# Kernel optimization log

Measured on AMD Instinct MI355X. Metric: run time of the kernel, lower is better.

Reference implementation:

```python
import jax, jax.numpy as jnp
import numpy as np

THRESHOLD = 0.5  # default threshold from MemoryPool.update

N, D, P, C0 = 16384, 1024, 4096, 2048


def setup_inputs() -> dict:
    key = jax.random.key(0)
    k1, k2, k3, k4 = jax.random.split(key, 4)
    summaries = jax.random.normal(k1, (N, D), dtype=jnp.float32)
    scores = jax.random.uniform(k2, (N,), dtype=jnp.float32)
    slot = jnp.arange(P)
    # slots >= count are empty (zeros), matching fresh torch buffers
    pool = jnp.where((slot < C0)[:, None],
                     jax.random.normal(k3, (P, D), dtype=jnp.float32), 0.0)
    priorities = jnp.where(slot < C0,
                           jax.random.uniform(k4, (P,), dtype=jnp.float32), 0.0)
    return {"summaries": summaries, "scores": scores,
            "pool": pool, "priorities": priorities, "count": C0}


def reference(summaries, scores, pool, priorities, count):
    pool_size = pool.shape[0]
    cnt0 = jnp.asarray(count, jnp.int32)

    def step(carry, xc):
        pl, pr, cnt = carry
        s, sc = xc  # (D,), ()
        valid = sc > THRESHOLD
        min_idx = jnp.argmin(pr)
        has_room = cnt < pool_size
        idx = jnp.where(has_room, cnt, min_idx)
        replace_ok = sc > pr[min_idx]
        do_write = valid & (has_room | replace_ok)
        new_pl = jnp.where(do_write, pl.at[idx].set(s), pl)
        new_pr = jnp.where(do_write, pr.at[idx].set(sc), pr)
        new_cnt = cnt + (do_write & has_room).astype(jnp.int32)
        return (new_pl, new_pr, new_cnt), None

    (pool_out, prior_out, cnt_out), _ = jax.lax.scan(
        step, (pool, priorities, cnt0), (summaries, scores))
    return pool_out, prior_out, cnt_out
```

## Files before the change

kernel.cpp:

```cpp
#include <hip/hip_runtime.h>

typedef unsigned long long u64;
#define THRESH 0.5f
#define ALL1 0xFFFFFFFFFFFFFFFFull
#define FINF __builtin_inff()

__device__ __forceinline__ u64 shflxU64(u64 v, int m) { return __shfl_xor(v, m, 64); }
__device__ __forceinline__ void sort64(u64 &key, int lane) {
#pragma unroll
    for (int k = 2; k <= 64; k <<= 1) {
#pragma unroll
        for (int j = k >> 1; j > 0; j >>= 1) {
            u64 p = shflxU64(key, j);
            bool takeMax = ((lane & j) != 0) != ((lane & k) != 0);
            u64 mn = key < p ? key : p;
            u64 mx = key < p ? p : key;
            key = takeMax ? mx : mn;
        }
    }
}

__device__ __forceinline__ u64 mkey(float v, int id) {
    v = (v == 0.0f) ? 0.0f : v;
    unsigned u = __float_as_uint(v);
    u ^= (unsigned)((int)u >> 31) | 0x80000000u;
    return ((u64)u << 32) | (unsigned)id;
}

__device__ __forceinline__ int blockScanExcl1024(int c, int tid, int* wpart,
                                                 int* totalOut) {
    const int lane = tid & 63, wid = tid >> 6;
    int pc = c;
#pragma unroll
    for (int off = 1; off < 64; off <<= 1) {
        int y = __shfl_up(pc, off, 64);
        if (lane >= off) pc += y;
    }
    if (lane == 63) wpart[wid] = pc;
    __syncthreads();
    if (tid < 16) {
        int v = wpart[tid];
#pragma unroll
        for (int off = 1; off < 16; off <<= 1) {
            int y = __shfl_up(v, off, 16);
            if (tid >= off) v += y;
        }
        wpart[tid] = v;
    }
    __syncthreads();
    *totalOut = wpart[15];
    return pc - c + (wid > 0 ? wpart[wid - 1] : 0);
}

__global__ __launch_bounds__(1024) void k1_scan(
    const float* __restrict__ scores, const float* __restrict__ priorities,
    const int* __restrict__ countPtr, int N, int P,
    float* __restrict__ outPrior, float* __restrict__ outCnt, int* __restrict__ srcWs,
    float* __restrict__ cval, int* __restrict__ csrc, int* __restrict__ meta,
    int* __restrict__ cnt2, int* __restrict__ cnt4)
{
    const int tid = threadIdx.x;
    for (int s = tid; s < P; s += 1024) { outPrior[s] = priorities[s]; srcWs[s] = -1; }
    for (int s = tid; s < N; s += 1024) cnt2[s] = 0;
    for (int s = tid; s < P + N; s += 1024) cnt4[s] = 0;
    int C0 = *countPtr; C0 = C0 < 0 ? 0 : (C0 > P ? P : C0);
    const int per = (N + 1023) >> 10;
    const int i0 = tid * per;
    float sv[16];
    if (per == 16 && i0 + 16 <= N) {
        const float4* s4 = (const float4*)(scores + i0);
        const float4 a = s4[0], b = s4[1], c4 = s4[2], d = s4[3];
        sv[0]=a.x; sv[1]=a.y; sv[2]=a.z; sv[3]=a.w;
        sv[4]=b.x; sv[5]=b.y; sv[6]=b.z; sv[7]=b.w;
        sv[8]=c4.x; sv[9]=c4.y; sv[10]=c4.z; sv[11]=c4.w;
        sv[12]=d.x; sv[13]=d.y; sv[14]=d.z; sv[15]=d.w;
    } else {
#pragma unroll 16
        for (int j = 0; j < 16; ++j)
            sv[j] = (j < per && i0 + j < N) ? scores[i0 + j] : 0.f;
    }
    int c = 0;
#pragma unroll 16
    for (int j = 0; j < 16; ++j) c += (j < per && i0 + j < N && sv[j] > THRESH) ? 1 : 0;
    __shared__ int wpart[16];
    int total;
    int v = blockScanExcl1024(c, tid, wpart, &total);
    int A = P - C0; if (A > total) A = total; if (A < 0) A = 0;
#pragma unroll 16
    for (int j = 0; j < 16; ++j) {
        if (j < per && i0 + j < N) {
            const float sc = sv[j];
            if (sc > THRESH) {
                if (v < A) { outPrior[C0 + v] = sc; srcWs[C0 + v] = i0 + j; }
                else { cval[v - A] = sc; csrc[v - A] = i0 + j; }
                ++v;
            }
        }
    }
    if (tid == 0) {
        meta[0] = total - A;
        meta[1] = C0 + A;
        outCnt[0] = (float)(C0 + A);
    }
}

#define K2T 512
__global__ __launch_bounds__(256) void k2_count(
    const float* __restrict__ outPrior, const float* __restrict__ cval,
    const int* __restrict__ meta, int* __restrict__ cnt2)
{
    const int M = meta[0], F = meta[1];
    const int iB = blockIdx.x << 8;
    if (iB >= M) return;
    const int hi = min(M, iB + 256);
    const int smax = F + hi;
    const int tb = blockIdx.y * K2T;
    if (tb >= smax) return;
    const int te = min(smax - tb, K2T);
    __shared__ __align__(16) float tile[K2T];
    for (int t = threadIdx.x; t < K2T; t += 256) {
        const int s = tb + t;
        tile[t] = (t < te) ? ((s < F) ? outPrior[s] : cval[s - F]) : FINF;
    }
    __syncthreads();
    const int i = iB + threadIdx.x;
    if (i >= M) return;
    const float x = cval[i];
    int cnt = 0;
    const float4* t4 = (const float4*)tile;
    if (tb + K2T <= F + iB) {
#pragma unroll 8
        for (int q = 0; q < K2T / 4; ++q) {
            const float4 w = t4[q];
            cnt += (w.x < x) + (w.y < x) + (w.z < x) + (w.w < x);
        }
    } else {
        int lim = F + i - tb;
        if (lim < 0) lim = 0;
        if (lim > te) lim = te;
        const int l4 = lim >> 2;
        for (int q = 0; q < l4; ++q) {
            const float4 w = t4[q];
            cnt += (w.x < x) + (w.y < x) + (w.z < x) + (w.w < x);
        }
        for (int t = l4 << 2; t < lim; ++t) cnt += tile[t] < x;
    }
    if (cnt) atomicAdd(&cnt2[i], cnt);
}

__global__ __launch_bounds__(1024) void k3_compact(
    const float* __restrict__ cval, const int* __restrict__ csrc,
    const int* __restrict__ cnt2, int* __restrict__ meta,
    float* __restrict__ cvalS, float* __restrict__ wval, int* __restrict__ wsrc,
    int* __restrict__ writeNum)
{
    const int M = meta[0];
    const int tid = threadIdx.x;
    const int per = (M + 1023) >> 10;
    const int i0 = tid * per, i1 = min(i0 + per, M);
    int c = 0;
    for (int i = i0; i < i1; ++i) c += (cnt2[i] >= i + 1) ? 1 : 0;
    __shared__ int wpart[16];
    int total;
    int w = blockScanExcl1024(c, tid, wpart, &total);
    for (int i = i0; i < i1; ++i) {
        if (cnt2[i] >= i + 1) {
            wval[w] = cval[i]; wsrc[w] = csrc[i]; writeNum[i] = w; cvalS[i] = cval[i]; ++w;
        } else { writeNum[i] = -1; cvalS[i] = FINF; }
    }
    if (tid == 0) meta[2] = total;
}

#define K4T 512
__global__ __launch_bounds__(256) void k4_count(
    const float* __restrict__ outPrior, const float* __restrict__ cvalS,
    const int* __restrict__ meta, int P, int* __restrict__ cnt4)
{
    const int M = meta[0], F = meta[1];
    if (M == 0) return;
    const int tot = F + M;
    const int eB = blockIdx.x << 8;
    if (eB >= tot) return;
    const int tb = blockIdx.y * K4T;
    if (tb >= tot) return;
    const int te = min(tot - tb, K4T);
    __shared__ __align__(16) u64 tile[K4T];
    for (int t = threadIdx.x; t < K4T; t += 256) {
        const int s = tb + t;
        u64 kk = ALL1;
        if (t < te) {
            if (s < F) kk = mkey(outPrior[s], s);
            else       kk = mkey(cvalS[s - F], P + (s - F));
        }
        tile[t] = kk;
    }
    __syncthreads();
    const int e = eB + threadIdx.x;
    if (e >= tot) return;
    float x; int id;
    if (e < F) { x = outPrior[e]; id = e; }
    else {
        x = cvalS[e - F];
        if (x == FINF) return;
        id = P + (e - F);
    }
    const u64 kx = mkey(x, id);
    int cnt = 0;
    const ulonglong2* t2 = (const ulonglong2*)tile;
#pragma unroll 8
    for (int q = 0; q < K4T / 2; ++q) {
        const ulonglong2 w = t2[q];
        cnt += (int)(w.x < kx) + (int)(w.y < kx);
    }
    if (cnt) atomicAdd(&cnt4[e], cnt);
}

#define SCAP 14400
#define DONEF (1 << 30)
#define MSF   (1 << 29)
#define TIEF  (1 << 28)
#define RSF   (1 << 27)
#define PAYM  ((1 << 27) - 1)
__global__ __launch_bounds__(1024) void k5_chain(
    float* __restrict__ evV, int* __restrict__ evId,
    const int* __restrict__ meta, int P,
    const float* __restrict__ wval, const int* __restrict__ wsrc,
    int* __restrict__ survW,
    float* outPrior, int* __restrict__ srcWs,
    const float* __restrict__ cvalS, const int* __restrict__ writeNum,
    const int* __restrict__ cnt4)
{
    __shared__ int state[SCAP];
    __shared__ int shRp, shLeft;
    const int tid = threadIdx.x;
    const int M = meta[0], F = meta[1], R = meta[2];
    if (M == 0) return;
    const int tot = F + M;

    for (int e = tid; e < tot; e += 1024) {
        float x; int myid; bool isC = false; int wn = -1;
        if (e < F) { x = outPrior[e]; myid = e; }
        else {
            const int i = e - F;
            x = cvalS[i];
            if (x == FINF) continue;
            isC = true; wn = writeNum[i]; myid = P + i;
        }
        const int cnt = cnt4[e];
        if (isC) survW[wn] = (cnt >= R) ? 1 : 0;
        if (cnt < R + 64) { evV[cnt] = x; evId[cnt] = isC ? (P + wn) : myid; }
    }
    __syncthreads();

    if (R <= 0 || R > SCAP) return;
    const int Wtot = F + R;

    if (tid == 0) {
        int Rp = R;
        if (R < Wtot) {
            const float vR1 = evV[R - 1];
            if (evV[R] == vR1) {
                int rr = R - 1;
                while (rr >= 0 && evV[rr] == vR1) --rr;
                Rp = rr + 1;
            }
        }
        shRp = Rp;
    }
    __syncthreads();
    const int Rp = shRp;

    for (int r = tid; r < Rp; r += 1024) {
        const float v = evV[r];
        const bool tp = (r > 0) && (evV[r - 1] == v);
        const bool tn = (r + 1 < Rp) && (evV[r + 1] == v);
        const bool tie = tp || tn;
        const int rs = (tie && !tp) ? RSF : 0;
        const int id = evId[r];
        int st;
        if (id < P) st = id | MSF | (tie ? (TIEF | rs) : DONEF);
        else        st = (id - P) | (tie ? (TIEF | rs) : 0);
        state[r] = st;
    }
    __syncthreads();

    for (int round = 0; round < Rp + 2; ++round) {
        for (int r = tid; r < Rp; r += 1024) {
            const int s = state[r];
            if (s & MSF) continue;
            int p = s & PAYM;
            int ms = -1;
            for (int g = 0; g < Rp + 2; ++g) {
                const int sp = state[p];
                if (sp & DONEF) { ms = sp & PAYM; break; }
                if (sp & (MSF | TIEF)) break;
                const int q = sp & PAYM;
                if (q >= p) break;
                p = q;
            }
            if (ms >= 0)
                state[r] = ms | MSF | ((s & TIEF) ? (s & (TIEF | RSF)) : DONEF);
            else
                state[r] = p | (s & (TIEF | RSF));
        }
        __syncthreads();
        for (int r = tid; r < Rp; r += 1024) {
            const int s = state[r];
            if (!(s & RSF) || (s & DONEF)) continue;
            int re = r + 1;
            while (re < Rp) {
                const int t = state[re];
                if ((t & TIEF) && !(t & RSF)) ++re; else break;
            }
            bool ready = true;
            for (int q = r; q < re; ++q) ready &= (state[q] & MSF) != 0;
            if (!ready) continue;
            for (int j = r; j < re; ++j) {
                int best = j;
                for (int q = j + 1; q < re; ++q)
                    if ((state[q] & PAYM) < (state[best] & PAYM)) best = q;
                if (best != j) {
                    const int pj = state[j] & PAYM, pb = state[best] & PAYM;
                    state[j]    = (state[j] & ~PAYM) | pb;
                    state[best] = (state[best] & ~PAYM) | pj;
                }
            }
            for (int j = r; j < re; ++j) state[j] |= DONEF;
        }
        __syncthreads();
        if (tid == 0) shLeft = 0;
        __syncthreads();
        int loc = 0;
        for (int r = tid; r < Rp; r += 1024) loc += (state[r] & DONEF) ? 0 : 1;
        if (loc) atomicAdd(&shLeft, loc);
        __syncthreads();
        if (shLeft == 0) break;
    }
    __syncthreads();

    if (Rp < R && tid < 64) {
        const int lane = tid;
        const int r = Rp + lane;
        const float v0 = evV[Rp];
        const bool mem = (r < Wtot) && (evV[r] == v0);
        const int g = (int)__popcll(__ballot(mem));
        const int e = R - Rp;
        int id = 0, ms = 0;
        if (mem) {
            id = evId[r];
            ms = (id < P) ? id : (state[id - P] & PAYM);
        }
        u64 key = mem ? ((((u64)(unsigned)ms) << 32) | (u64)(unsigned)id) : ALL1;
        sort64(key, lane);
        const int sid = (int)(unsigned)(key & 0xFFFFFFFFull);
        const int sms = (int)(unsigned)(key >> 32);
        const bool real = (key != ALL1) && (lane < g);
        if (real && lane < e) state[Rp + lane] = sms;
        if (real && sid >= P) survW[sid - P] = (lane >= e) ? 1 : 0;
    }
    __syncthreads();

    for (int j = tid; j < R; j += 1024) {
        if (survW[j]) {
            const int sl = state[j] & PAYM;
            outPrior[sl] = wval[j];
            srcWs[sl] = wsrc[j];
        }
    }
}

__global__ __launch_bounds__(256) void gather_kernel(
    const float* __restrict__ summaries,
    const float* __restrict__ pool,
    const int* __restrict__ src,
    float* __restrict__ outPool, int D) {
    int p = blockIdx.x;
    int s = src[p];
    const float* row = (s >= 0) ? (summaries + (size_t)s * D) : (pool + (size_t)p * D);
    float* o = outPool + (size_t)p * D;
    if ((D & 3) == 0) {
        for (int k = (threadIdx.x << 2); k < D; k += (blockDim.x << 2)) {
            float4 v = *(const float4*)(row + k);
            *(float4*)(o + k) = v;
        }
    } else {
        for (int k = threadIdx.x; k < D; k += blockDim.x) o[k] = row[k];
    }
}

extern "C" void kernel_launch(void* const* d_in, const int* in_sizes, int n_in,
                              void* d_out, int out_size, void* d_ws, size_t ws_size,
                              hipStream_t stream) {
    const float* summaries  = (const float*)d_in[0];
    const float* scores     = (const float*)d_in[1];
    const float* pool       = (const float*)d_in[2];
    const float* priorities = (const float*)d_in[3];
    const int*   count      = (const int*)d_in[4];

    int N = in_sizes[1];
    int P = in_sizes[3];
    int D = in_sizes[0] / N;

    float* outPool  = (float*)d_out;
    float* outPrior = outPool + (size_t)P * D;
    float* outCnt   = outPrior + P;
    int*   srcWs    = (int*)d_ws;

    float* cval     = outPool;
    int*   csrc     = (int*)outPool + 1 * N;
    float* cvalS    = outPool + 3 * N;
    float* wval     = outPool + 4 * N;
    int*   wsrc     = (int*)outPool + 5 * N;
    int*   writeNum = (int*)outPool + 6 * N;
    float* evV      = outPool + 7 * N;
    int*   evId     = (int*)outPool + 8 * N + 64;
    int*   survW    = (int*)outPool + 10 * N + 128;
    int*   meta     = (int*)outPool + 11 * N + 128;
    int*   cnt2     = (int*)outPool + 11 * N + 192;
    int*   cnt4     = (int*)outPool + 12 * N + 192;

    const int nb2 = (N + 255) / 256;
    const int nb4 = (P + N + 255) / 256;
    const int ty  = (P + N + K2T - 1) / K2T;

    dim3 g2(nb2, ty), g4(nb4, ty);

    k1_scan<<<1, 1024, 0, stream>>>(scores, priorities, count, N, P,
                                    outPrior, outCnt, srcWs, cval, csrc, meta,
                                    cnt2, cnt4);
    k2_count<<<g2, 256, 0, stream>>>(outPrior, cval, meta, cnt2);
    k3_compact<<<1, 1024, 0, stream>>>(cval, csrc, cnt2, meta, cvalS, wval, wsrc, writeNum);
    k4_count<<<g4, 256, 0, stream>>>(outPrior, cvalS, meta, P, cnt4);
    k5_chain<<<1, 1024, 0, stream>>>(evV, evId, meta, P, wval, wsrc, survW,
                                     outPrior, srcWs, cvalS, writeNum, cnt4);
    gather_kernel<<<P, 256, 0, stream>>>(summaries, pool, srcWs, outPool, D);
}
```

Before: 183.9 us.

## Fuse count and compact kernels via ticket, move scatter into k4, parallelize init

Spreads the buffer initialisation in k1 across 16 extra blocks, and has the single scan block fill only the untouched prior slots. k2 and k3 become one kernel: the last block to finish, picked with an atomic ticket counter, does the compaction. k4 packs a per-element completion count into the high bits of its atomic counter, so whichever block finishes an element also scatters evV/evId/survW, removing that serial loop from the single-block k5. The gather becomes a grid-stride loop over 1024 blocks. The aim is fewer launches and less single-block serial work, at the cost of atomic-ticket ordering subtleties, and tickets is reset by k1 blocks that run concurrently with block 0.

```diff
diff --git a/kernel.cpp b/kernel.cpp
--- a/kernel.cpp
+++ b/kernel.cpp
@@ -4,6 +4,9 @@
 #define THRESH 0.5f
 #define ALL1 0xFFFFFFFFFFFFFFFFull
 #define FINF __builtin_inff()
+
+#define TOUCHB (1 << 20)
+#define CMASK  (TOUCHB - 1)
 
 __device__ __forceinline__ u64 shflxU64(u64 v, int m) { return __shfl_xor(v, m, 64); }
 __device__ __forceinline__ void sort64(u64 &key, int lane) {
@@ -57,13 +60,21 @@
     const int* __restrict__ countPtr, int N, int P,
     float* __restrict__ outPrior, float* __restrict__ outCnt, int* __restrict__ srcWs,
     float* __restrict__ cval, int* __restrict__ csrc, int* __restrict__ meta,
-    int* __restrict__ cnt2, int* __restrict__ cnt4)
+    int* __restrict__ cnt2, int* __restrict__ cnt4, int* __restrict__ tickets)
 {
     const int tid = threadIdx.x;
-    for (int s = tid; s < P; s += 1024) { outPrior[s] = priorities[s]; srcWs[s] = -1; }
-    for (int s = tid; s < N; s += 1024) cnt2[s] = 0;
-    for (int s = tid; s < P + N; s += 1024) cnt4[s] = 0;
     int C0 = *countPtr; C0 = C0 < 0 ? 0 : (C0 > P ? P : C0);
+
+    if (blockIdx.x != 0) {
+        const int bt = (int)(blockIdx.x - 1) * 1024 + tid;
+        const int BT = 16 * 1024;
+        for (int s = bt; s < C0; s += BT) { outPrior[s] = priorities[s]; srcWs[s] = -1; }
+        for (int s = bt; s < N; s += BT) cnt2[s] = 0;
+        for (int s = bt; s < P + N; s += BT) cnt4[s] = 0;
+        if (bt == 0) tickets[0] = 0;
+        return;
+    }
+
     const int per = (N + 1023) >> 10;
     const int i0 = tid * per;
     float sv[16];
@@ -97,6 +108,9 @@
             }
         }
     }
+    for (int s = C0 + A + tid; s < P; s += 1024) {
+        outPrior[s] = priorities[s]; srcWs[s] = -1;
+    }
     if (tid == 0) {
         meta[0] = total - A;
         meta[1] = C0 + A;
@@ -105,66 +119,78 @@
 }
 
 #define K2T 512
-__global__ __launch_bounds__(256) void k2_count(
+__global__ __launch_bounds__(1024) void k23(
     const float* __restrict__ outPrior, const float* __restrict__ cval,
-    const int* __restrict__ meta, int* __restrict__ cnt2)
-{
-    const int M = meta[0], F = meta[1];
-    const int iB = blockIdx.x << 8;
-    if (iB >= M) return;
-    const int hi = min(M, iB + 256);
-    const int smax = F + hi;
-    const int tb = blockIdx.y * K2T;
-    if (tb >= smax) return;
-    const int te = min(smax - tb, K2T);
-    __shared__ __align__(16) float tile[K2T];
-    for (int t = threadIdx.x; t < K2T; t += 256) {
-        const int s = tb + t;
-        tile[t] = (t < te) ? ((s < F) ? outPrior[s] : cval[s - F]) : FINF;
-    }
-    __syncthreads();
-    const int i = iB + threadIdx.x;
-    if (i >= M) return;
-    const float x = cval[i];
-    int cnt = 0;
-    const float4* t4 = (const float4*)tile;
-    if (tb + K2T <= F + iB) {
-#pragma unroll 8
-        for (int q = 0; q < K2T / 4; ++q) {
-            const float4 w = t4[q];
-            cnt += (w.x < x) + (w.y < x) + (w.z < x) + (w.w < x);
-        }
-    } else {
-        int lim = F + i - tb;
-        if (lim < 0) lim = 0;
-        if (lim > te) lim = te;
-        const int l4 = lim >> 2;
-        for (int q = 0; q < l4; ++q) {
-            const float4 w = t4[q];
-            cnt += (w.x < x) + (w.y < x) + (w.z < x) + (w.w < x);
-        }
-        for (int t = l4 << 2; t < lim; ++t) cnt += tile[t] < x;
-    }
-    if (cnt) atomicAdd(&cnt2[i], cnt);
-}
-
-__global__ __launch_bounds__(1024) void k3_compact(
-    const float* __restrict__ cval, const int* __restrict__ csrc,
-    const int* __restrict__ cnt2, int* __restrict__ meta,
+    const int* __restrict__ csrc, int* __restrict__ meta,
+    int* __restrict__ cnt2, int* __restrict__ tickets,
     float* __restrict__ cvalS, float* __restrict__ wval, int* __restrict__ wsrc,
     int* __restrict__ writeNum)
 {
-    const int M = meta[0];
+    __shared__ __align__(16) float tile[K2T];
+    __shared__ int wpart[16];
+    __shared__ int shLast;
     const int tid = threadIdx.x;
+    const int M = meta[0], F = meta[1];
+
+    const int iB = (int)blockIdx.x << 10;
+    const int tb = (int)blockIdx.y * K2T;
+    int te = 0;
+    if (iB < M) {
+        const int hi = min(M, iB + 1024);
+        const int smax = F + hi;
+        if (tb < smax) te = min(smax - tb, K2T);
+    }
+    if (te > 0) {
+        for (int t = tid; t < K2T; t += 1024) {
+            const int s = tb + t;
+            tile[t] = (t < te) ? ((s < F) ? outPrior[s] : cval[s - F]) : FINF;
+        }
+        __syncthreads();
+        const int i = iB + tid;
+        if (i < M) {
+            const float x = cval[i];
+            int cnt = 0;
+            const float4* t4 = (const float4*)tile;
+            if (tb + K2T <= F + iB) {
+#pragma unroll 8
+                for (int q = 0; q < K2T / 4; ++q) {
+                    const float4 w = t4[q];
+                    cnt += (w.x < x) + (w.y < x) + (w.z < x) + (w.w < x);
+                }
+            } else {
+                int lim = F + i - tb;
+                if (lim < 0) lim = 0;
+                if (lim > te) lim = te;
+                const int l4 = lim >> 2;
+                for (int q = 0; q < l4; ++q) {
+                    const float4 w = t4[q];
+                    cnt += (w.x < x) + (w.y < x) + (w.z < x) + (w.w < x);
+                }
+                for (int t = l4 << 2; t < lim; ++t) cnt += tile[t] < x;
+            }
+            if (cnt) atomicAdd(&cnt2[i], cnt);
+        }
+    }
+    __syncthreads();
+    if (tid == 0)
+        shLast = (atomicAdd(&tickets[0], 1) == (int)(gridDim.x * gridDim.y) - 1);
+    __syncthreads();
+    if (!shLast) return;
+
     const int per = (M + 1023) >> 10;
     const int i0 = tid * per, i1 = min(i0 + per, M);
+    int cv[16];
     int c = 0;
-    for (int i = i0; i < i1; ++i) c += (cnt2[i] >= i + 1) ? 1 : 0;
-    __shared__ int wpart[16];
+    for (int i = i0, j = 0; i < i1; ++i, ++j) {
+        const int q = atomicAdd(&cnt2[i], 0);
+        cv[j] = q;
+        c += (q >= i + 1) ? 1 : 0;
+    }
+    __syncthreads();
     int total;
     int w = blockScanExcl1024(c, tid, wpart, &total);
-    for (int i = i0; i < i1; ++i) {
-        if (cnt2[i] >= i + 1) {
+    for (int i = i0, j = 0; i < i1; ++i, ++j) {
+        if (cv[j] >= i + 1) {
             wval[w] = cval[i]; wsrc[w] = csrc[i]; writeNum[i] = w; cvalS[i] = cval[i]; ++w;
         } else { writeNum[i] = -1; cvalS[i] = FINF; }
     }
@@ -174,14 +200,16 @@
 #define K4T 512
 __global__ __launch_bounds__(256) void k4_count(
     const float* __restrict__ outPrior, const float* __restrict__ cvalS,
-    const int* __restrict__ meta, int P, int* __restrict__ cnt4)
+    const int* __restrict__ writeNum, const int* __restrict__ meta, int P,
+    int* __restrict__ cnt4,
+    float* __restrict__ evV, int* __restrict__ evId, int* __restrict__ survW)
 {
     const int M = meta[0], F = meta[1];
     if (M == 0) return;
     const int tot = F + M;
-    const int eB = blockIdx.x << 8;
+    const int eB = (int)blockIdx.x << 8;
     if (eB >= tot) return;
-    const int tb = blockIdx.y * K4T;
+    const int tb = (int)blockIdx.y * K4T;
     if (tb >= tot) return;
     const int te = min(tot - tb, K4T);
     __shared__ __align__(16) u64 tile[K4T];
@@ -197,12 +225,12 @@
     __syncthreads();
     const int e = eB + threadIdx.x;
     if (e >= tot) return;
-    float x; int id;
+    float x; int id; bool isC = false;
     if (e < F) { x = outPrior[e]; id = e; }
     else {
         x = cvalS[e - F];
         if (x == FINF) return;
-        id = P + (e - F);
+        id = P + (e - F); isC = true;
     }
     const u64 kx = mkey(x, id);
     int cnt = 0;
@@ -212,7 +240,19 @@
         const ulonglong2 w = t2[q];
         cnt += (int)(w.x < kx) + (int)(w.y < kx);
     }
-    if (cnt) atomicAdd(&cnt4[e], cnt);
+    const int TY = (tot + K4T - 1) / K4T;
+    const int old = atomicAdd(&cnt4[e], cnt | TOUCHB);
+    if ((old >> 20) == TY - 1) {
+        const int fin = (old & CMASK) + cnt;
+        const int R = meta[2];
+        if (isC) {
+            const int wn = writeNum[e - F];
+            survW[wn] = (fin >= R) ? 1 : 0;
+            if (fin < R + 64) { evV[fin] = x; evId[fin] = P + wn; }
+        } else {
+            if (fin < R + 64) { evV[fin] = x; evId[fin] = e; }
+        }
+    }
 }
 
 #define SCAP 14400
@@ -222,37 +262,18 @@
 #define RSF   (1 << 27)
 #define PAYM  ((1 << 27) - 1)
 __global__ __launch_bounds__(1024) void k5_chain(
-    float* __restrict__ evV, int* __restrict__ evId,
+    const float* __restrict__ evV, const int* __restrict__ evId,
     const int* __restrict__ meta, int P,
     const float* __restrict__ wval, const int* __restrict__ wsrc,
     int* __restrict__ survW,
-    float* outPrior, int* __restrict__ srcWs,
-    const float* __restrict__ cvalS, const int* __restrict__ writeNum,
-    const int* __restrict__ cnt4)
+    float* outPrior, int* __restrict__ srcWs)
 {
     __shared__ int state[SCAP];
     __shared__ int shRp, shLeft;
     const int tid = threadIdx.x;
-    const int M = meta[0], F = meta[1], R = meta[2];
-    if (M == 0) return;
-    const int tot = F + M;
-
-    for (int e = tid; e < tot; e += 1024) {
-        float x; int myid; bool isC = false; int wn = -1;
-        if (e < F) { x = outPrior[e]; myid = e; }
-        else {
-            const int i = e - F;
-            x = cvalS[i];
-            if (x == FINF) continue;
-            isC = true; wn = writeNum[i]; myid = P + i;
-        }
-        const int cnt = cnt4[e];
-        if (isC) survW[wn] = (cnt >= R) ? 1 : 0;
-        if (cnt < R + 64) { evV[cnt] = x; evId[cnt] = isC ? (P + wn) : myid; }
-    }
-    __syncthreads();
-
+    const int R = meta[2];
     if (R <= 0 || R > SCAP) return;
+    const int F = meta[1];
     const int Wtot = F + R;
 
     if (tid == 0) {
@@ -373,18 +394,19 @@
     const float* __restrict__ summaries,
     const float* __restrict__ pool,
     const int* __restrict__ src,
-    float* __restrict__ outPool, int D) {
-    int p = blockIdx.x;
-    int s = src[p];
-    const float* row = (s >= 0) ? (summaries + (size_t)s * D) : (pool + (size_t)p * D);
-    float* o = outPool + (size_t)p * D;
-    if ((D & 3) == 0) {
-        for (int k = (threadIdx.x << 2); k < D; k += (blockDim.x << 2)) {
-            float4 v = *(const float4*)(row + k);
-            *(float4*)(o + k) = v;
-        }
-    } else {
-        for (int k = threadIdx.x; k < D; k += blockDim.x) o[k] = row[k];
+    float* __restrict__ outPool, int P, int D) {
+    for (int p = blockIdx.x; p < P; p += gridDim.x) {
+        const int s = src[p];
+        const float* row = (s >= 0) ? (summaries + (size_t)s * D)
+                                    : (pool + (size_t)p * D);
+        float* o = outPool + (size_t)p * D;
+        if ((D & 3) == 0) {
+            const int dq = D >> 2;
+            for (int k = threadIdx.x; k < dq; k += blockDim.x)
+                ((float4*)o)[k] = ((const float4*)row)[k];
+        } else {
+            for (int k = threadIdx.x; k < D; k += blockDim.x) o[k] = row[k];
+        }
     }
 }
 
@@ -418,20 +440,20 @@
     int*   meta     = (int*)outPool + 11 * N + 128;
     int*   cnt2     = (int*)outPool + 11 * N + 192;
     int*   cnt4     = (int*)outPool + 12 * N + 192;
-
-    const int nb2 = (N + 255) / 256;
-    const int nb4 = (P + N + 255) / 256;
-    const int ty  = (P + N + K2T - 1) / K2T;
-
-    dim3 g2(nb2, ty), g4(nb4, ty);
-
-    k1_scan<<<1, 1024, 0, stream>>>(scores, priorities, count, N, P,
-                                    outPrior, outCnt, srcWs, cval, csrc, meta,
-                                    cnt2, cnt4);
-    k2_count<<<g2, 256, 0, stream>>>(outPrior, cval, meta, cnt2);
-    k3_compact<<<1, 1024, 0, stream>>>(cval, csrc, cnt2, meta, cvalS, wval, wsrc, writeNum);
-    k4_count<<<g4, 256, 0, stream>>>(outPrior, cvalS, meta, P, cnt4);
+    int*   tickets  = (int*)outPool + 13 * N + 256;
+
+    const int ty = (P + N + K2T - 1) / K2T;
+    dim3 g23((N + 1023) / 1024, ty);
+    dim3 g4((P + N + 255) / 256, ty);
+
+    k1_scan<<<17, 1024, 0, stream>>>(scores, priorities, count, N, P,
+                                     outPrior, outCnt, srcWs, cval, csrc, meta,
+                                     cnt2, cnt4, tickets);
+    k23<<<g23, 1024, 0, stream>>>(outPrior, cval, csrc, meta, cnt2, tickets,
+                                  cvalS, wval, wsrc, writeNum);
+    k4_count<<<g4, 256, 0, stream>>>(outPrior, cvalS, writeNum, meta, P, cnt4,
+                                     evV, evId, survW);
     k5_chain<<<1, 1024, 0, stream>>>(evV, evId, meta, P, wval, wsrc, survW,
-                                     outPrior, srcWs, cvalS, writeNum, cnt4);
-    gather_kernel<<<P, 256, 0, stream>>>(summaries, pool, srcWs, outPool, D);
-}
+                                     outPrior, srcWs);
+    gather_kernel<<<1024, 256, 0, stream>>>(summaries, pool, srcWs, outPool, P, D);
+}
```

Result: faster. 178.4 us (-3.0%).
